# Optimization experiments

Measured on AMD Instinct MI355X. Metric: run time of the kernel, lower is better.

The kernel has to match this reference:

```python
import jax, jax.numpy as jnp
import numpy as np

B, T, C = 4, 2048, 1024
H = 16
D = C // H  # 64


def setup_inputs() -> dict:
    key = jax.random.key(0)
    ks = jax.random.split(key, 6)
    s = 1.0 / np.sqrt(C)
    return {
        "x": jax.random.normal(ks[0], (B, T, C), dtype=jnp.float32),
        "W_q": jax.random.uniform(ks[1], (C, C), dtype=jnp.float32, minval=-s, maxval=s),
        "W_k": jax.random.uniform(ks[2], (C, C), dtype=jnp.float32, minval=-s, maxval=s),
        "W_v": jax.random.uniform(ks[3], (C, C), dtype=jnp.float32, minval=-s, maxval=s),
        "W_o": jax.random.uniform(ks[4], (C, C), dtype=jnp.float32, minval=-s, maxval=s),
        "b_o": jax.random.uniform(ks[5], (C,), dtype=jnp.float32, minval=-s, maxval=s),
    }


def reference(x, W_q, W_k, W_v, W_o, b_o):
    b, t, c = x.shape
    # project and split heads: (B, H, T, D)
    def heads(w):
        return (x @ w).reshape(b, t, H, D).transpose(0, 2, 1, 3)
    Q, K, V = heads(W_q), heads(W_k), heads(W_v)
    scale = 1.0 / np.sqrt(D).astype(np.float32)
    scores = jnp.einsum('bhqd,bhkd->bhqk', Q, K) * scale  # (B,H,T,T)
    # causal mask: True above diagonal -> masked out
    causal = jnp.triu(jnp.ones((t, t), dtype=bool), k=1)
    scores = jnp.where(causal, -jnp.inf, scores)
    weights = jax.nn.softmax(scores, axis=-1)
    ctx = jnp.einsum('bhqk,bhkd->bhqd', weights, V)
    ctx = ctx.transpose(0, 2, 1, 3).reshape(b, t, c)
    return ctx @ W_o + b_o
```

## Files before the change

### kernel.cpp

```cpp
#include <hip/hip_runtime.h>
#include <math.h>
#include <stdint.h>

#define TSEQ 2048
#define NB   4
#define CD   1024
#define NH   16
#define HD   64
#define MR   8192

typedef __bf16 bf16x8 __attribute__((ext_vector_type(8)));
typedef float  f32x4  __attribute__((ext_vector_type(4)));
typedef float  f32x16 __attribute__((ext_vector_type(16)));

__device__ __forceinline__ unsigned short f2b(float f) {
  unsigned u = __float_as_uint(f);
  u += 0x7fffu + ((u >> 16) & 1u);
  return (unsigned short)(u >> 16);
}
__device__ __forceinline__ unsigned cvtpk(float lo, float hi) {
  unsigned r;
  asm("v_cvt_pk_bf16_f32 %0, %1, %2" : "=v"(r) : "v"(lo), "v"(hi));
  return r;
}

__device__ __forceinline__ void gll16(const void* g, const void* l) {
  __builtin_amdgcn_global_load_lds(
      (const __attribute__((address_space(1))) unsigned*)(uintptr_t)g,
      (__attribute__((address_space(3))) unsigned*)(uintptr_t)l, 16, 0, 0);
}

__global__ __launch_bounds__(256) void cast_x_k(const float* __restrict__ in,
                                                unsigned short* __restrict__ out) {
  int i = blockIdx.x * 256 + threadIdx.x;
  const float4* p = (const float4*)in;
  float4 a = p[2 * i], b = p[2 * i + 1];
  uint4 o;
  o.x = f2b(a.x) | ((unsigned)f2b(a.y) << 16);
  o.y = f2b(a.z) | ((unsigned)f2b(a.w) << 16);
  o.z = f2b(b.x) | ((unsigned)f2b(b.y) << 16);
  o.w = f2b(b.z) | ((unsigned)f2b(b.w) << 16);
  ((uint4*)out)[i] = o;
}

__global__ __launch_bounds__(256) void castT_k(
    const float* __restrict__ w0, const float* __restrict__ w1,
    const float* __restrict__ w2, const float* __restrict__ w3,
    unsigned short* __restrict__ o0, unsigned short* __restrict__ o1,
    unsigned short* __restrict__ o2, unsigned short* __restrict__ o3) {
  const float* W = blockIdx.z == 0 ? w0 : blockIdx.z == 1 ? w1 : blockIdx.z == 2 ? w2 : w3;
  unsigned short* O = blockIdx.z == 0 ? o0 : blockIdx.z == 1 ? o1 : blockIdx.z == 2 ? o2 : o3;
  __shared__ float t[32][33];
  int tx = threadIdx.x & 31, ty = threadIdx.x >> 5;
  #pragma unroll
  for (int i = 0; i < 4; ++i)
    t[ty + i * 8][tx] = W[(size_t)(blockIdx.y * 32 + ty + i * 8) * CD + blockIdx.x * 32 + tx];
  __syncthreads();
  #pragma unroll
  for (int i = 0; i < 4; ++i)
    O[(size_t)(blockIdx.x * 32 + ty + i * 8) * CD + blockIdx.y * 32 + tx] = f2b(t[tx][ty + i * 8]);
}

template <int MODE>
__global__ __launch_bounds__(256) void gemm_k(const unsigned short* __restrict__ A,
                                              const unsigned short* __restrict__ Bt,
                                              void* __restrict__ o0, void* __restrict__ o1,
                                              void* __restrict__ o2,
                                              const float* __restrict__ bias) {
  __shared__ __align__(16) unsigned short Asl[128 * 32];
  __shared__ __align__(16) unsigned short Bsl[128 * 32];
  const int tid = threadIdx.x, lane = tid & 63, w = tid >> 6;
  const int li = lane & 15, lg = lane >> 4;
  const int bm = blockIdx.x, bn = blockIdx.y;
  const int wr = w >> 1, wc = w & 1;

  f32x4 acc[4][4];
  #pragma unroll
  for (int mi = 0; mi < 4; ++mi)
    #pragma unroll
    for (int ni = 0; ni < 4; ++ni) acc[mi][ni] = (f32x4){0.f, 0.f, 0.f, 0.f};

  for (int kt = 0; kt < 32; ++kt) {
    #pragma unroll
    for (int it = 0; it < 2; ++it) {
      int c = (w * 2 + it) * 64 + lane;
      int r = c >> 2, ko = (c & 3) * 8;
      gll16(A  + (size_t)(bm * 128 + r) * CD + kt * 32 + ko, (const char*)Asl + (w * 2 + it) * 1024);
      gll16(Bt + (size_t)(bn * 128 + r) * CD + kt * 32 + ko, (const char*)Bsl + (w * 2 + it) * 1024);
    }
    __syncthreads();
    bf16x8 af[4], bfr[4];
    #pragma unroll
    for (int mi = 0; mi < 4; ++mi)
      af[mi] = *(const bf16x8*)&Asl[(wr * 64 + mi * 16 + li) * 32 + lg * 8];
    #pragma unroll
    for (int ni = 0; ni < 4; ++ni)
      bfr[ni] = *(const bf16x8*)&Bsl[(wc * 64 + ni * 16 + li) * 32 + lg * 8];
    #pragma unroll
    for (int mi = 0; mi < 4; ++mi)
      #pragma unroll
      for (int ni = 0; ni < 4; ++ni)
        acc[mi][ni] = __builtin_amdgcn_mfma_f32_16x16x32_bf16(af[mi], bfr[ni], acc[mi][ni], 0, 0, 0);
    __syncthreads();
  }

  #pragma unroll
  for (int mi = 0; mi < 4; ++mi)
    #pragma unroll
    for (int ni = 0; ni < 4; ++ni)
      #pragma unroll
      for (int r = 0; r < 4; ++r) {
        int row = bm * 128 + wr * 64 + mi * 16 + lg * 4 + r;
        int col = bn * 128 + wc * 64 + ni * 16 + li;
        float v = acc[mi][ni][r];
        if constexpr (MODE == 3) {
          int seg = col >> 10, c2 = col & 1023;
          if (seg == 0) {
            ((unsigned short*)o0)[(size_t)row * CD + c2] = f2b(v);
          } else if (seg == 1) {
            ((unsigned short*)o1)[(size_t)row * CD + c2] = f2b(v);
          } else {
            int b = row >> 11, t = row & 2047;
            ((unsigned short*)o2)[(size_t)(b * CD + c2) * TSEQ + t] = f2b(v);
          }
        } else {
          ((float*)o0)[(size_t)row * CD + col] = v + bias[col];
        }
      }
}

__global__ __launch_bounds__(256) void attn_k(const unsigned short* __restrict__ Qm,
                                              const unsigned short* __restrict__ Km,
                                              const unsigned short* __restrict__ Vt,
                                              unsigned short* __restrict__ Cx) {
  __shared__ __align__(16) unsigned short Kt[2][2048];
  __shared__ __align__(16) unsigned short Vs[2][2048];
  const int tid = threadIdx.x, w = tid >> 6, lane = tid & 63;
  const int q32 = lane & 31, hi = lane >> 5;
  const int pj = blockIdx.x, bh = blockIdx.y;
  const int b = bh >> 4, h = bh & 15;
  const float SC = 0.18033688011112042f;

  #pragma unroll 1
  for (int pass = 0; pass < 2; ++pass) {
    const int qt = pass ? (15 - pj) : pj;
    const int qloc = qt * 128 + w * 32 + q32;
    const size_t qrow = (size_t)(b * TSEQ) + qloc;
    const int NKB = qt * 4 + 4;
    const int diag = qt * 4 + w;

    bf16x8 qf[4];
    #pragma unroll
    for (int dc = 0; dc < 4; ++dc)
      qf[dc] = *(const bf16x8*)&Qm[qrow * CD + h * 64 + dc * 16 + hi * 8];

    f32x16 oc0, oc1;
    #pragma unroll
    for (int r = 0; r < 16; ++r) { oc0[r] = 0.f; oc1[r] = 0.f; }
    float m = -INFINITY, lsum = 0.f;

    auto stage = [&](int kb, int buf) {
      gll16(Km + (size_t)(b * TSEQ + kb * 32 + q32) * CD + h * 64 + w * 16 + hi * 8,
            (const char*)&Kt[buf][w * 512]);
      gll16(Vt + ((size_t)b * CD + h * 64 + (w & 1) * 32 + q32) * TSEQ + kb * 32 + (w >> 1) * 16 + hi * 8,
            (const char*)&Vs[buf][w * 512]);
    };

    stage(0, 0);
    #pragma unroll 1
    for (int kb = 0; kb < NKB; ++kb) {
      const int buf = kb & 1;
      if (kb + 1 < NKB) {
        stage(kb + 1, buf ^ 1);
        asm volatile("s_waitcnt vmcnt(2)" ::: "memory");
      } else {
        asm volatile("s_waitcnt vmcnt(0)" ::: "memory");
      }
      __builtin_amdgcn_s_barrier();
      __builtin_amdgcn_sched_barrier(0);

      f32x16 st;
      #pragma unroll
      for (int r = 0; r < 16; ++r) st[r] = 0.f;
      #pragma unroll
      for (int dc = 0; dc < 4; ++dc) {
        bf16x8 kf = *(const bf16x8*)&Kt[buf][dc * 512 + lane * 8];
        st = __builtin_amdgcn_mfma_f32_32x32x16_bf16(kf, qf[dc], st, 0, 0, 0);
      }

      if (kb >= diag) {
        #pragma unroll
        for (int r = 0; r < 16; ++r) {
          int kloc = kb * 32 + (r & 3) + 8 * (r >> 2) + 4 * hi;
          if (kloc > qloc) st[r] = -INFINITY;
        }
      }

      float rmax = st[0];
      #pragma unroll
      for (int r = 1; r < 16; ++r) rmax = fmaxf(rmax, st[r]);
      rmax = fmaxf(rmax, __shfl_xor(rmax, 32));
      float mnew = fmaxf(m, rmax);
      float alpha = exp2f((m - mnew) * SC);
      float p[16], psum = 0.f;
      #pragma unroll
      for (int r = 0; r < 16; ++r) {
        p[r] = exp2f((st[r] - mnew) * SC);
        psum += p[r];
      }
      psum += __shfl_xor(psum, 32);
      lsum = lsum * alpha + psum;
      m = mnew;
      #pragma unroll
      for (int r = 0; r < 16; ++r) { oc0[r] *= alpha; oc1[r] *= alpha; }

      unsigned W[4][2], X[4][2];
      #pragma unroll
      for (int s = 0; s < 4; ++s)
        #pragma unroll
        for (int t = 0; t < 2; ++t) W[s][t] = cvtpk(p[4 * s + 2 * t], p[4 * s + 2 * t + 1]);
      #pragma unroll
      for (int s = 0; s < 4; ++s)
        #pragma unroll
        for (int t = 0; t < 2; ++t) X[s][t] = __shfl_xor(W[s][t], 32);

      const bool h1 = (hi == 1);
      uint4 pw0, pw1;
      pw0.x = h1 ? X[1][0] : W[0][0];
      pw0.y = h1 ? X[1][1] : W[0][1];
      pw0.z = h1 ? W[1][0] : X[0][0];
      pw0.w = h1 ? W[1][1] : X[0][1];
      pw1.x = h1 ? X[3][0] : W[2][0];
      pw1.y = h1 ? X[3][1] : W[2][1];
      pw1.z = h1 ? W[3][0] : X[2][0];
      pw1.w = h1 ? W[3][1] : X[2][1];
      bf16x8 pb0 = *(bf16x8*)&pw0, pb1 = *(bf16x8*)&pw1;

      {
        bf16x8 v00 = *(const bf16x8*)&Vs[buf][(0 * 2 + 0) * 512 + lane * 8];
        bf16x8 v01 = *(const bf16x8*)&Vs[buf][(0 * 2 + 1) * 512 + lane * 8];
        bf16x8 v10 = *(const bf16x8*)&Vs[buf][(1 * 2 + 0) * 512 + lane * 8];
        bf16x8 v11 = *(const bf16x8*)&Vs[buf][(1 * 2 + 1) * 512 + lane * 8];
        oc0 = __builtin_amdgcn_mfma_f32_32x32x16_bf16(v00, pb0, oc0, 0, 0, 0);
        oc1 = __builtin_amdgcn_mfma_f32_32x32x16_bf16(v01, pb0, oc1, 0, 0, 0);
        oc0 = __builtin_amdgcn_mfma_f32_32x32x16_bf16(v10, pb1, oc0, 0, 0, 0);
        oc1 = __builtin_amdgcn_mfma_f32_32x32x16_bf16(v11, pb1, oc1, 0, 0, 0);
      }
      asm volatile("s_waitcnt lgkmcnt(0)" ::: "memory");
      __builtin_amdgcn_s_barrier();
    }

    float inv = 1.f / lsum;
    #pragma unroll
    for (int dh = 0; dh < 2; ++dh)
      #pragma unroll
      for (int g = 0; g < 4; ++g) {
        ushort4 sv;
        float v0 = (dh ? oc1[4 * g + 0] : oc0[4 * g + 0]) * inv;
        float v1 = (dh ? oc1[4 * g + 1] : oc0[4 * g + 1]) * inv;
        float v2 = (dh ? oc1[4 * g + 2] : oc0[4 * g + 2]) * inv;
        float v3 = (dh ? oc1[4 * g + 3] : oc0[4 * g + 3]) * inv;
        sv.x = f2b(v0); sv.y = f2b(v1); sv.z = f2b(v2); sv.w = f2b(v3);
        *(ushort4*)&Cx[qrow * CD + h * 64 + dh * 32 + 8 * g + 4 * hi] = sv;
      }
  }
}

extern "C" void kernel_launch(void* const* d_in, const int* in_sizes, int n_in,
                              void* d_out, int out_size, void* d_ws, size_t ws_size,
                              hipStream_t stream) {
  const float* x  = (const float*)d_in[0];
  const float* Wq = (const float*)d_in[1];
  const float* Wk = (const float*)d_in[2];
  const float* Wv = (const float*)d_in[3];
  const float* Wo = (const float*)d_in[4];
  const float* bo = (const float*)d_in[5];
  float* out = (float*)d_out;

  char* W = (char*)d_ws;
  unsigned short* xb  = (unsigned short*)(W);
  unsigned short* WqT = (unsigned short*)(W + (16u << 20));
  unsigned short* WkT = (unsigned short*)(W + (18u << 20));
  unsigned short* WvT = (unsigned short*)(W + (20u << 20));
  unsigned short* WoT = (unsigned short*)(W + (22u << 20));
  unsigned short* Qm  = (unsigned short*)(W + (24u << 20));
  unsigned short* Km  = (unsigned short*)(W + (40u << 20));
  unsigned short* Vt  = (unsigned short*)(W + (56u << 20));
  unsigned short* Cx  = (unsigned short*)(W + (72u << 20));

  hipLaunchKernelGGL(cast_x_k, dim3(4096), dim3(256), 0, stream, x, xb);
  hipLaunchKernelGGL(castT_k, dim3(32, 32, 4), dim3(256), 0, stream,
                     Wq, Wk, Wv, Wo, WqT, WkT, WvT, WoT);
  hipLaunchKernelGGL((gemm_k<3>), dim3(64, 24), dim3(256), 0, stream,
                     xb, WqT, (void*)Qm, (void*)Km, (void*)Vt, (const float*)nullptr);
  hipLaunchKernelGGL(attn_k, dim3(8, 64), dim3(256), 0, stream, Qm, Km, Vt, Cx);
  hipLaunchKernelGGL((gemm_k<2>), dim3(64, 8), dim3(256), 0, stream,
                     Cx, WoT, (void*)out, nullptr, nullptr, bo);
}
```

Baseline: 306.9 us.

## Double-buffer GEMM tiles, swizzle block order, lazy softmax rescale in attention

The GEMM kernel gets two LDS buffers, so the next K-tile's global-to-LDS load is issued before the current tile's MFMAs. Workgroup IDs are remapped so neighbouring tiles share the same XCD. The attention kernel drops the paired two-pass-per-block scheme: it launches one block per query tile, heaviest tiles first, with a swizzled mapping. It also skips the running-max rescale of the accumulators unless the max grows by more than a threshold, which saves ALU work per key block. In exchange, LDS use in the GEMM doubles, and the unnormalised probabilities can reach larger magnitudes in bf16.

```diff
diff --git a/kernel.cpp b/kernel.cpp
--- a/kernel.cpp
+++ b/kernel.cpp
@@ -67,11 +67,14 @@
                                               void* __restrict__ o0, void* __restrict__ o1,
                                               void* __restrict__ o2,
                                               const float* __restrict__ bias) {
-  __shared__ __align__(16) unsigned short Asl[128 * 32];
-  __shared__ __align__(16) unsigned short Bsl[128 * 32];
+  __shared__ __align__(16) unsigned short Asl[2][128 * 32];
+  __shared__ __align__(16) unsigned short Bsl[2][128 * 32];
   const int tid = threadIdx.x, lane = tid & 63, w = tid >> 6;
   const int li = lane & 15, lg = lane >> 4;
-  const int bm = blockIdx.x, bn = blockIdx.y;
+  const int nwg = gridDim.x * gridDim.y;
+  const int bid = blockIdx.y * gridDim.x + blockIdx.x;
+  const int swz = (bid & 7) * (nwg >> 3) + (bid >> 3);
+  const int bm = swz & 63, bn = swz >> 6;
   const int wr = w >> 1, wc = w & 1;
 
   f32x4 acc[4][4];
@@ -80,22 +83,32 @@
     #pragma unroll
     for (int ni = 0; ni < 4; ++ni) acc[mi][ni] = (f32x4){0.f, 0.f, 0.f, 0.f};
 
-  for (int kt = 0; kt < 32; ++kt) {
+  auto stage = [&](int kt, int buf) {
     #pragma unroll
     for (int it = 0; it < 2; ++it) {
       int c = (w * 2 + it) * 64 + lane;
       int r = c >> 2, ko = (c & 3) * 8;
-      gll16(A  + (size_t)(bm * 128 + r) * CD + kt * 32 + ko, (const char*)Asl + (w * 2 + it) * 1024);
-      gll16(Bt + (size_t)(bn * 128 + r) * CD + kt * 32 + ko, (const char*)Bsl + (w * 2 + it) * 1024);
-    }
-    __syncthreads();
+      gll16(A  + (size_t)(bm * 128 + r) * CD + kt * 32 + ko,
+            (const char*)Asl[buf] + (w * 2 + it) * 1024);
+      gll16(Bt + (size_t)(bn * 128 + r) * CD + kt * 32 + ko,
+            (const char*)Bsl[buf] + (w * 2 + it) * 1024);
+    }
+  };
+
+  stage(0, 0);
+  __syncthreads();
+
+  #pragma unroll 2
+  for (int kt = 0; kt < 32; ++kt) {
+    const int buf = kt & 1;
+    if (kt + 1 < 32) stage(kt + 1, buf ^ 1);
     bf16x8 af[4], bfr[4];
     #pragma unroll
     for (int mi = 0; mi < 4; ++mi)
-      af[mi] = *(const bf16x8*)&Asl[(wr * 64 + mi * 16 + li) * 32 + lg * 8];
+      af[mi] = *(const bf16x8*)&Asl[buf][(wr * 64 + mi * 16 + li) * 32 + lg * 8];
     #pragma unroll
     for (int ni = 0; ni < 4; ++ni)
-      bfr[ni] = *(const bf16x8*)&Bsl[(wc * 64 + ni * 16 + li) * 32 + lg * 8];
+      bfr[ni] = *(const bf16x8*)&Bsl[buf][(wc * 64 + ni * 16 + li) * 32 + lg * 8];
     #pragma unroll
     for (int mi = 0; mi < 4; ++mi)
       #pragma unroll
@@ -137,133 +150,140 @@
   __shared__ __align__(16) unsigned short Vs[2][2048];
   const int tid = threadIdx.x, w = tid >> 6, lane = tid & 63;
   const int q32 = lane & 31, hi = lane >> 5;
-  const int pj = blockIdx.x, bh = blockIdx.y;
+  const int bid = blockIdx.x;
+  const int swz = (bid & 7) * 128 + (bid >> 3);
+  const int bh = swz >> 4, qi = swz & 15;
+  const int qt = 15 - qi;
   const int b = bh >> 4, h = bh & 15;
   const float SC = 0.18033688011112042f;
 
+  const int qloc = qt * 128 + w * 32 + q32;
+  const size_t qrow = (size_t)(b * TSEQ) + qloc;
+  const int NKB = qt * 4 + 4;
+  const int diag = qt * 4 + w;
+
+  bf16x8 qf[4];
+  #pragma unroll
+  for (int dc = 0; dc < 4; ++dc)
+    qf[dc] = *(const bf16x8*)&Qm[qrow * CD + h * 64 + dc * 16 + hi * 8];
+
+  f32x16 oc0, oc1;
+  #pragma unroll
+  for (int r = 0; r < 16; ++r) { oc0[r] = 0.f; oc1[r] = 0.f; }
+  float m = -INFINITY, lsum = 0.f;
+
+  auto stage = [&](int kb, int buf) {
+    gll16(Km + (size_t)(b * TSEQ + kb * 32 + q32) * CD + h * 64 + w * 16 + hi * 8,
+          (const char*)&Kt[buf][w * 512]);
+    gll16(Vt + ((size_t)b * CD + h * 64 + (w & 1) * 32 + q32) * TSEQ + kb * 32 + (w >> 1) * 16 + hi * 8,
+          (const char*)&Vs[buf][w * 512]);
+  };
+
+  stage(0, 0);
   #pragma unroll 1
-  for (int pass = 0; pass < 2; ++pass) {
-    const int qt = pass ? (15 - pj) : pj;
-    const int qloc = qt * 128 + w * 32 + q32;
-    const size_t qrow = (size_t)(b * TSEQ) + qloc;
-    const int NKB = qt * 4 + 4;
-    const int diag = qt * 4 + w;
-
-    bf16x8 qf[4];
-    #pragma unroll
-    for (int dc = 0; dc < 4; ++dc)
-      qf[dc] = *(const bf16x8*)&Qm[qrow * CD + h * 64 + dc * 16 + hi * 8];
-
-    f32x16 oc0, oc1;
-    #pragma unroll
-    for (int r = 0; r < 16; ++r) { oc0[r] = 0.f; oc1[r] = 0.f; }
-    float m = -INFINITY, lsum = 0.f;
-
-    auto stage = [&](int kb, int buf) {
-      gll16(Km + (size_t)(b * TSEQ + kb * 32 + q32) * CD + h * 64 + w * 16 + hi * 8,
-            (const char*)&Kt[buf][w * 512]);
-      gll16(Vt + ((size_t)b * CD + h * 64 + (w & 1) * 32 + q32) * TSEQ + kb * 32 + (w >> 1) * 16 + hi * 8,
-            (const char*)&Vs[buf][w * 512]);
-    };
-
-    stage(0, 0);
-    #pragma unroll 1
-    for (int kb = 0; kb < NKB; ++kb) {
-      const int buf = kb & 1;
-      if (kb + 1 < NKB) {
-        stage(kb + 1, buf ^ 1);
-        asm volatile("s_waitcnt vmcnt(2)" ::: "memory");
-      } else {
-        asm volatile("s_waitcnt vmcnt(0)" ::: "memory");
+  for (int kb = 0; kb < NKB; ++kb) {
+    const int buf = kb & 1;
+    if (kb + 1 < NKB) {
+      stage(kb + 1, buf ^ 1);
+      asm volatile("s_waitcnt vmcnt(2)" ::: "memory");
+    } else {
+      asm volatile("s_waitcnt vmcnt(0)" ::: "memory");
+    }
+    __builtin_amdgcn_s_barrier();
+    __builtin_amdgcn_sched_barrier(0);
+
+    f32x16 st;
+    #pragma unroll
+    for (int r = 0; r < 16; ++r) st[r] = 0.f;
+    #pragma unroll
+    for (int dc = 0; dc < 4; ++dc) {
+      bf16x8 kf = *(const bf16x8*)&Kt[buf][dc * 512 + lane * 8];
+      st = __builtin_amdgcn_mfma_f32_32x32x16_bf16(kf, qf[dc], st, 0, 0, 0);
+    }
+
+    if (kb >= diag) {
+      #pragma unroll
+      for (int r = 0; r < 16; ++r) {
+        int kloc = kb * 32 + (r & 3) + 8 * (r >> 2) + 4 * hi;
+        if (kloc > qloc) st[r] = -INFINITY;
       }
-      __builtin_amdgcn_s_barrier();
-      __builtin_amdgcn_sched_barrier(0);
-
-      f32x16 st;
-      #pragma unroll
-      for (int r = 0; r < 16; ++r) st[r] = 0.f;
-      #pragma unroll
-      for (int dc = 0; dc < 4; ++dc) {
-        bf16x8 kf = *(const bf16x8*)&Kt[buf][dc * 512 + lane * 8];
-        st = __builtin_amdgcn_mfma_f32_32x32x16_bf16(kf, qf[dc], st, 0, 0, 0);
-      }
-
-      if (kb >= diag) {
-        #pragma unroll
-        for (int r = 0; r < 16; ++r) {
-          int kloc = kb * 32 + (r & 3) + 8 * (r >> 2) + 4 * hi;
-          if (kloc > qloc) st[r] = -INFINITY;
-        }
-      }
-
-      float rmax = st[0];
-      #pragma unroll
-      for (int r = 1; r < 16; ++r) rmax = fmaxf(rmax, st[r]);
-      rmax = fmaxf(rmax, __shfl_xor(rmax, 32));
+    }
+
+    float m01 = fmaxf(st[0], st[1]),  m23 = fmaxf(st[2], st[3]);
+    float m45 = fmaxf(st[4], st[5]),  m67 = fmaxf(st[6], st[7]);
+    float m89 = fmaxf(st[8], st[9]),  mab = fmaxf(st[10], st[11]);
+    float mcd = fmaxf(st[12], st[13]), mef = fmaxf(st[14], st[15]);
+    float rmax = fmaxf(fmaxf(fmaxf(m01, m23), fmaxf(m45, m67)),
+                       fmaxf(fmaxf(m89, mab), fmaxf(mcd, mef)));
+    rmax = fmaxf(rmax, __shfl_xor(rmax, 32));
+
+    if (!__all((rmax - m) * SC <= 8.f)) {
       float mnew = fmaxf(m, rmax);
       float alpha = exp2f((m - mnew) * SC);
-      float p[16], psum = 0.f;
-      #pragma unroll
-      for (int r = 0; r < 16; ++r) {
-        p[r] = exp2f((st[r] - mnew) * SC);
-        psum += p[r];
-      }
-      psum += __shfl_xor(psum, 32);
-      lsum = lsum * alpha + psum;
+      lsum *= alpha;
+      #pragma unroll
+      for (int r = 0; r < 16; ++r) { oc0[r] *= alpha; oc1[r] *= alpha; }
       m = mnew;
-      #pragma unroll
-      for (int r = 0; r < 16; ++r) { oc0[r] *= alpha; oc1[r] *= alpha; }
-
-      unsigned W[4][2], X[4][2];
-      #pragma unroll
-      for (int s = 0; s < 4; ++s)
-        #pragma unroll
-        for (int t = 0; t < 2; ++t) W[s][t] = cvtpk(p[4 * s + 2 * t], p[4 * s + 2 * t + 1]);
-      #pragma unroll
-      for (int s = 0; s < 4; ++s)
-        #pragma unroll
-        for (int t = 0; t < 2; ++t) X[s][t] = __shfl_xor(W[s][t], 32);
-
-      const bool h1 = (hi == 1);
-      uint4 pw0, pw1;
-      pw0.x = h1 ? X[1][0] : W[0][0];
-      pw0.y = h1 ? X[1][1] : W[0][1];
-      pw0.z = h1 ? W[1][0] : X[0][0];
-      pw0.w = h1 ? W[1][1] : X[0][1];
-      pw1.x = h1 ? X[3][0] : W[2][0];
-      pw1.y = h1 ? X[3][1] : W[2][1];
-      pw1.z = h1 ? W[3][0] : X[2][0];
-      pw1.w = h1 ? W[3][1] : X[2][1];
-      bf16x8 pb0 = *(bf16x8*)&pw0, pb1 = *(bf16x8*)&pw1;
-
-      {
-        bf16x8 v00 = *(const bf16x8*)&Vs[buf][(0 * 2 + 0) * 512 + lane * 8];
-        bf16x8 v01 = *(const bf16x8*)&Vs[buf][(0 * 2 + 1) * 512 + lane * 8];
-        bf16x8 v10 = *(const bf16x8*)&Vs[buf][(1 * 2 + 0) * 512 + lane * 8];
-        bf16x8 v11 = *(const bf16x8*)&Vs[buf][(1 * 2 + 1) * 512 + lane * 8];
-        oc0 = __builtin_amdgcn_mfma_f32_32x32x16_bf16(v00, pb0, oc0, 0, 0, 0);
-        oc1 = __builtin_amdgcn_mfma_f32_32x32x16_bf16(v01, pb0, oc1, 0, 0, 0);
-        oc0 = __builtin_amdgcn_mfma_f32_32x32x16_bf16(v10, pb1, oc0, 0, 0, 0);
-        oc1 = __builtin_amdgcn_mfma_f32_32x32x16_bf16(v11, pb1, oc1, 0, 0, 0);
-      }
-      asm volatile("s_waitcnt lgkmcnt(0)" ::: "memory");
-      __builtin_amdgcn_s_barrier();
-    }
-
-    float inv = 1.f / lsum;
-    #pragma unroll
-    for (int dh = 0; dh < 2; ++dh)
-      #pragma unroll
-      for (int g = 0; g < 4; ++g) {
-        ushort4 sv;
-        float v0 = (dh ? oc1[4 * g + 0] : oc0[4 * g + 0]) * inv;
-        float v1 = (dh ? oc1[4 * g + 1] : oc0[4 * g + 1]) * inv;
-        float v2 = (dh ? oc1[4 * g + 2] : oc0[4 * g + 2]) * inv;
-        float v3 = (dh ? oc1[4 * g + 3] : oc0[4 * g + 3]) * inv;
-        sv.x = f2b(v0); sv.y = f2b(v1); sv.z = f2b(v2); sv.w = f2b(v3);
-        *(ushort4*)&Cx[qrow * CD + h * 64 + dh * 32 + 8 * g + 4 * hi] = sv;
-      }
+    }
+
+    float p[16], psum = 0.f;
+    #pragma unroll
+    for (int r = 0; r < 16; ++r) {
+      p[r] = exp2f((st[r] - m) * SC);
+      psum += p[r];
+    }
+    psum += __shfl_xor(psum, 32);
+    lsum += psum;
+
+    unsigned W[4][2], X[4][2];
+    #pragma unroll
+    for (int s = 0; s < 4; ++s)
+      #pragma unroll
+      for (int t = 0; t < 2; ++t) W[s][t] = cvtpk(p[4 * s + 2 * t], p[4 * s + 2 * t + 1]);
+    #pragma unroll
+    for (int s = 0; s < 4; ++s)
+      #pragma unroll
+      for (int t = 0; t < 2; ++t) X[s][t] = __shfl_xor(W[s][t], 32);
+
+    const bool h1 = (hi == 1);
+    uint4 pw0, pw1;
+    pw0.x = h1 ? X[1][0] : W[0][0];
+    pw0.y = h1 ? X[1][1] : W[0][1];
+    pw0.z = h1 ? W[1][0] : X[0][0];
+    pw0.w = h1 ? W[1][1] : X[0][1];
+    pw1.x = h1 ? X[3][0] : W[2][0];
+    pw1.y = h1 ? X[3][1] : W[2][1];
+    pw1.z = h1 ? W[3][0] : X[2][0];
+    pw1.w = h1 ? W[3][1] : X[2][1];
+    bf16x8 pb0 = *(bf16x8*)&pw0, pb1 = *(bf16x8*)&pw1;
+
+    {
+      bf16x8 v00 = *(const bf16x8*)&Vs[buf][(0 * 2 + 0) * 512 + lane * 8];
+      bf16x8 v01 = *(const bf16x8*)&Vs[buf][(0 * 2 + 1) * 512 + lane * 8];
+      bf16x8 v10 = *(const bf16x8*)&Vs[buf][(1 * 2 + 0) * 512 + lane * 8];
+      bf16x8 v11 = *(const bf16x8*)&Vs[buf][(1 * 2 + 1) * 512 + lane * 8];
+      oc0 = __builtin_amdgcn_mfma_f32_32x32x16_bf16(v00, pb0, oc0, 0, 0, 0);
+      oc1 = __builtin_amdgcn_mfma_f32_32x32x16_bf16(v01, pb0, oc1, 0, 0, 0);
+      oc0 = __builtin_amdgcn_mfma_f32_32x32x16_bf16(v10, pb1, oc0, 0, 0, 0);
+      oc1 = __builtin_amdgcn_mfma_f32_32x32x16_bf16(v11, pb1, oc1, 0, 0, 0);
+    }
+    asm volatile("s_waitcnt lgkmcnt(0)" ::: "memory");
+    __builtin_amdgcn_s_barrier();
   }
+
+  float inv = 1.f / lsum;
+  #pragma unroll
+  for (int dh = 0; dh < 2; ++dh)
+    #pragma unroll
+    for (int g = 0; g < 4; ++g) {
+      ushort4 sv;
+      float v0 = (dh ? oc1[4 * g + 0] : oc0[4 * g + 0]) * inv;
+      float v1 = (dh ? oc1[4 * g + 1] : oc0[4 * g + 1]) * inv;
+      float v2 = (dh ? oc1[4 * g + 2] : oc0[4 * g + 2]) * inv;
+      float v3 = (dh ? oc1[4 * g + 3] : oc0[4 * g + 3]) * inv;
+      sv.x = f2b(v0); sv.y = f2b(v1); sv.z = f2b(v2); sv.w = f2b(v3);
+      *(ushort4*)&Cx[qrow * CD + h * 64 + dh * 32 + 8 * g + 4 * hi] = sv;
+    }
 }
 
 extern "C" void kernel_launch(void* const* d_in, const int* in_sizes, int n_in,
@@ -293,7 +313,7 @@
                      Wq, Wk, Wv, Wo, WqT, WkT, WvT, WoT);
   hipLaunchKernelGGL((gemm_k<3>), dim3(64, 24), dim3(256), 0, stream,
                      xb, WqT, (void*)Qm, (void*)Km, (void*)Vt, (const float*)nullptr);
-  hipLaunchKernelGGL(attn_k, dim3(8, 64), dim3(256), 0, stream, Qm, Km, Vt, Cx);
+  hipLaunchKernelGGL(attn_k, dim3(1024), dim3(256), 0, stream, Qm, Km, Vt, Cx);
   hipLaunchKernelGGL((gemm_k<2>), dim3(64, 8), dim3(256), 0, stream,
                      Cx, WoT, (void*)out, nullptr, nullptr, bo);
 }
```

New measurement: 363.1 us. +18.3%, slower.

## Give each attention wave private K/V staging, per-wave causal trip count, lazy rescale

Applied to the files above, without the earlier changes.

Each wave now stages its own full K and V tile into a private LDS slice, so the block-wide barriers are gone and each wave stops at its own diagonal key block instead of the block's last one. Online softmax skips the max update and accumulator rescale unless the running max grows past a threshold, which saves exp and multiply work. The grid is flattened and remapped so blocks of the same tile position are spread across heads. In exchange LDS per block and global loads per wave both quadruple, since each wave reloads K/V that were shared before. The lazy rescale lets exponentials reach up to 2^8 before renormalising.

```diff
diff --git a/kernel.cpp b/kernel.cpp
--- a/kernel.cpp
+++ b/kernel.cpp
@@ -133,11 +133,12 @@
                                               const unsigned short* __restrict__ Km,
                                               const unsigned short* __restrict__ Vt,
                                               unsigned short* __restrict__ Cx) {
-  __shared__ __align__(16) unsigned short Kt[2][2048];
-  __shared__ __align__(16) unsigned short Vs[2][2048];
+  __shared__ __align__(16) unsigned short L[4][2][8][512];
   const int tid = threadIdx.x, w = tid >> 6, lane = tid & 63;
   const int q32 = lane & 31, hi = lane >> 5;
-  const int pj = blockIdx.x, bh = blockIdx.y;
+  const int bid = blockIdx.x;
+  const int bh = (bid & 7) * 8 + (bid >> 6);
+  const int pj = (bid >> 3) & 7;
   const int b = bh >> 4, h = bh & 15;
   const float SC = 0.18033688011112042f;
 
@@ -146,8 +147,8 @@
     const int qt = pass ? (15 - pj) : pj;
     const int qloc = qt * 128 + w * 32 + q32;
     const size_t qrow = (size_t)(b * TSEQ) + qloc;
-    const int NKB = qt * 4 + 4;
     const int diag = qt * 4 + w;
+    const int NKB = diag + 1;
 
     bf16x8 qf[4];
     #pragma unroll
@@ -160,10 +161,15 @@
     float m = -INFINITY, lsum = 0.f;
 
     auto stage = [&](int kb, int buf) {
-      gll16(Km + (size_t)(b * TSEQ + kb * 32 + q32) * CD + h * 64 + w * 16 + hi * 8,
-            (const char*)&Kt[buf][w * 512]);
-      gll16(Vt + ((size_t)b * CD + h * 64 + (w & 1) * 32 + q32) * TSEQ + kb * 32 + (w >> 1) * 16 + hi * 8,
-            (const char*)&Vs[buf][w * 512]);
+      const char* base = (const char*)&L[w][buf][0][0];
+      #pragma unroll
+      for (int dc = 0; dc < 4; ++dc)
+        gll16(Km + (size_t)(b * TSEQ + kb * 32 + q32) * CD + h * 64 + dc * 16 + hi * 8,
+              base + dc * 1024);
+      #pragma unroll
+      for (int f = 0; f < 4; ++f)
+        gll16(Vt + ((size_t)b * CD + h * 64 + (f & 1) * 32 + q32) * TSEQ + kb * 32 + (f >> 1) * 16 + hi * 8,
+              base + (4 + f) * 1024);
     };
 
     stage(0, 0);
@@ -172,23 +178,21 @@
       const int buf = kb & 1;
       if (kb + 1 < NKB) {
         stage(kb + 1, buf ^ 1);
-        asm volatile("s_waitcnt vmcnt(2)" ::: "memory");
+        asm volatile("s_waitcnt vmcnt(8)" ::: "memory");
       } else {
         asm volatile("s_waitcnt vmcnt(0)" ::: "memory");
       }
-      __builtin_amdgcn_s_barrier();
-      __builtin_amdgcn_sched_barrier(0);
 
       f32x16 st;
       #pragma unroll
       for (int r = 0; r < 16; ++r) st[r] = 0.f;
       #pragma unroll
       for (int dc = 0; dc < 4; ++dc) {
-        bf16x8 kf = *(const bf16x8*)&Kt[buf][dc * 512 + lane * 8];
+        bf16x8 kf = *(const bf16x8*)&L[w][buf][dc][lane * 8];
         st = __builtin_amdgcn_mfma_f32_32x32x16_bf16(kf, qf[dc], st, 0, 0, 0);
       }
 
-      if (kb >= diag) {
+      if (kb == diag) {
         #pragma unroll
         for (int r = 0; r < 16; ++r) {
           int kloc = kb * 32 + (r & 3) + 8 * (r >> 2) + 4 * hi;
@@ -196,23 +200,31 @@
         }
       }
 
-      float rmax = st[0];
-      #pragma unroll
-      for (int r = 1; r < 16; ++r) rmax = fmaxf(rmax, st[r]);
+      float m01 = fmaxf(st[0], st[1]),  m23 = fmaxf(st[2], st[3]);
+      float m45 = fmaxf(st[4], st[5]),  m67 = fmaxf(st[6], st[7]);
+      float m89 = fmaxf(st[8], st[9]),  mab = fmaxf(st[10], st[11]);
+      float mcd = fmaxf(st[12], st[13]), mef = fmaxf(st[14], st[15]);
+      float rmax = fmaxf(fmaxf(fmaxf(m01, m23), fmaxf(m45, m67)),
+                         fmaxf(fmaxf(m89, mab), fmaxf(mcd, mef)));
       rmax = fmaxf(rmax, __shfl_xor(rmax, 32));
-      float mnew = fmaxf(m, rmax);
-      float alpha = exp2f((m - mnew) * SC);
+
+      if (!__all((rmax - m) * SC <= 8.f)) {
+        float mnew = fmaxf(m, rmax);
+        float alpha = exp2f((m - mnew) * SC);
+        lsum *= alpha;
+        #pragma unroll
+        for (int r = 0; r < 16; ++r) { oc0[r] *= alpha; oc1[r] *= alpha; }
+        m = mnew;
+      }
+
       float p[16], psum = 0.f;
       #pragma unroll
       for (int r = 0; r < 16; ++r) {
-        p[r] = exp2f((st[r] - mnew) * SC);
+        p[r] = exp2f((st[r] - m) * SC);
         psum += p[r];
       }
       psum += __shfl_xor(psum, 32);
-      lsum = lsum * alpha + psum;
-      m = mnew;
-      #pragma unroll
-      for (int r = 0; r < 16; ++r) { oc0[r] *= alpha; oc1[r] *= alpha; }
+      lsum += psum;
 
       unsigned W[4][2], X[4][2];
       #pragma unroll
@@ -237,17 +249,15 @@
       bf16x8 pb0 = *(bf16x8*)&pw0, pb1 = *(bf16x8*)&pw1;
 
       {
-        bf16x8 v00 = *(const bf16x8*)&Vs[buf][(0 * 2 + 0) * 512 + lane * 8];
-        bf16x8 v01 = *(const bf16x8*)&Vs[buf][(0 * 2 + 1) * 512 + lane * 8];
-        bf16x8 v10 = *(const bf16x8*)&Vs[buf][(1 * 2 + 0) * 512 + lane * 8];
-        bf16x8 v11 = *(const bf16x8*)&Vs[buf][(1 * 2 + 1) * 512 + lane * 8];
+        bf16x8 v00 = *(const bf16x8*)&L[w][buf][4 + 0][lane * 8];
+        bf16x8 v01 = *(const bf16x8*)&L[w][buf][4 + 1][lane * 8];
+        bf16x8 v10 = *(const bf16x8*)&L[w][buf][4 + 2][lane * 8];
+        bf16x8 v11 = *(const bf16x8*)&L[w][buf][4 + 3][lane * 8];
         oc0 = __builtin_amdgcn_mfma_f32_32x32x16_bf16(v00, pb0, oc0, 0, 0, 0);
         oc1 = __builtin_amdgcn_mfma_f32_32x32x16_bf16(v01, pb0, oc1, 0, 0, 0);
         oc0 = __builtin_amdgcn_mfma_f32_32x32x16_bf16(v10, pb1, oc0, 0, 0, 0);
         oc1 = __builtin_amdgcn_mfma_f32_32x32x16_bf16(v11, pb1, oc1, 0, 0, 0);
       }
-      asm volatile("s_waitcnt lgkmcnt(0)" ::: "memory");
-      __builtin_amdgcn_s_barrier();
     }
 
     float inv = 1.f / lsum;
@@ -293,7 +303,7 @@
                      Wq, Wk, Wv, Wo, WqT, WkT, WvT, WoT);
   hipLaunchKernelGGL((gemm_k<3>), dim3(64, 24), dim3(256), 0, stream,
                      xb, WqT, (void*)Qm, (void*)Km, (void*)Vt, (const float*)nullptr);
-  hipLaunchKernelGGL(attn_k, dim3(8, 64), dim3(256), 0, stream, Qm, Km, Vt, Cx);
+  hipLaunchKernelGGL(attn_k, dim3(512), dim3(256), 0, stream, Qm, Km, Vt, Cx);
   hipLaunchKernelGGL((gemm_k<2>), dim3(64, 8), dim3(256), 0, stream,
                      Cx, WoT, (void*)out, nullptr, nullptr, bo);
 }
```

Measured after the change: 329.8 us. 7.5% more time.
